# Optimization experiments

Measured on AMD Instinct MI355X. Metric: run time of the kernel, lower is better.

The kernel has to match this reference:

```python
import jax, jax.numpy as jnp
import numpy as np
import itertools

B, K, H, W = 64, 5, 320, 320
EPS = 1e-6
# All K! permutations (exact equivalent of scipy.linear_sum_assignment for KxK cost)
PERMS = np.array(list(itertools.permutations(range(K))), dtype=np.int32)  # [P, K]


def setup_inputs() -> dict:
    key = jax.random.key(0)
    k1, k2, k3 = jax.random.split(key, 3)
    return {
        "fg_logits": jax.random.normal(k1, (B, 1, H, W), dtype=jnp.float32),
        "slot_logits": jax.random.normal(k2, (B, K, H, W), dtype=jnp.float32),
        "target": jax.random.uniform(k3, (B, 1, H, W), dtype=jnp.float32),
    }


def reference(fg_logits, slot_logits, target):
    fg = target[:, 0]            # [B,H,W]
    bg = 1.0 - fg                # [B,H,W]
    # targets_b: index 0 = FG mask, 1..K-1 = BG mask (duplicated)  -> [B,K,H,W]
    targets = jnp.concatenate([fg[:, None], jnp.broadcast_to(bg[:, None], (B, K - 1, H, W))], axis=1)

    # IoU cost matrix on detached sigmoid probs (matches .detach())
    probs = jax.lax.stop_gradient(jax.nn.sigmoid(slot_logits))
    s = probs.reshape(B, K, -1)        # [B,K,N]
    t = targets.reshape(B, K, -1)      # [B,K,N]
    inter = jnp.einsum('bkn,bjn->bkj', s, t)           # [B,K,K]
    union = s.sum(-1)[:, :, None] + t.sum(-1)[:, None, :] - inter + EPS
    cost = 1.0 - inter / union                          # [B,K,K]

    # Exact Hungarian via brute force over K! permutations (K small)
    perms = jnp.asarray(PERMS)                          # [P,K]
    rows = jnp.arange(K)[None, :]                       # [1,K]
    perm_cost = cost[:, rows, perms].sum(-1)            # [B,P]
    best_perm = perms[jnp.argmin(perm_cost, axis=1)]    # [B,K] col_ind per sample

    # aligned[i] = targets[col_ind[i]]; targets[j] is fg iff j == 0
    is_fg = (best_perm == 0)[:, :, None, None]          # [B,K,1,1]
    aligned = jnp.where(is_fg, fg[:, None], bg[:, None])  # [B,K,H,W]

    # Stable sigmoid-BCE with logits, mean-reduced per sample then averaged over B
    x = slot_logits
    bce = jnp.maximum(x, 0.0) - x * aligned + jnp.log1p(jnp.exp(-jnp.abs(x)))
    return bce.mean()
```

## Files before the change

kernel.cpp:

```cpp
#include <hip/hip_runtime.h>


#define BB 64
#define KK 5
#define NPIX 102400
#define QUARTERS 4
#define SEG 25600
#define ITERS 25
#define THREADS 256
#define REC 8
#define NBLK (BB * KK * QUARTERS)

__global__ void hung_pass1(const float* __restrict__ slot,
                           const float* __restrict__ tgt,
                           float* __restrict__ ws)
{
    const int bid = blockIdx.x;
    const int q   = bid & (QUARTERS - 1);
    const int bk  = bid >> 2;
    const int b   = bk / KK;

    const float* xk = slot + (size_t)bk * NPIX + q * SEG;
    const float* t  = tgt  + (size_t)b  * NPIX + q * SEG;

    float X = 0.f, XF = 0.f, S = 0.f, SF = 0.f, PX = 0.f, Tf = 0.f;

    const int base = threadIdx.x * 4;
    #pragma unroll 5
    for (int i = 0; i < ITERS; ++i) {
        const int off = base + i * (THREADS * 4);
        const float4 fg4 = *reinterpret_cast<const float4*>(t  + off);
        const float4 x4  = *reinterpret_cast<const float4*>(xk + off);
        const float fgv[4] = {fg4.x, fg4.y, fg4.z, fg4.w};
        const float xv[4]  = {x4.x, x4.y, x4.z, x4.w};
        #pragma unroll
        for (int j = 0; j < 4; ++j) {
            const float x  = xv[j];
            const float fg = fgv[j];
            const float e  = __expf(-fabsf(x));
            const float L  = __logf(1.0f + e);
            const float d  = L + fmaxf(-x, 0.0f);
            const float s  = __expf(-d);
            PX += d;
            X  += x;
            XF  = fmaf(x, fg, XF);
            S  += s;
            SF  = fmaf(s, fg, SF);
            Tf += fg;
        }
    }

    float v[6] = {X, XF, S, SF, PX, Tf};
    #pragma unroll
    for (int j = 0; j < 6; ++j) {
        float x = v[j];
        #pragma unroll
        for (int off = 32; off > 0; off >>= 1) x += __shfl_down(x, off, 64);
        v[j] = x;
    }
    __shared__ float red[THREADS / 64][6];
    const int lane = threadIdx.x & 63;
    const int w    = threadIdx.x >> 6;
    if (lane == 0) {
        #pragma unroll
        for (int j = 0; j < 6; ++j) red[w][j] = v[j];
    }
    __syncthreads();
    if (threadIdx.x < 6) {
        const int j = threadIdx.x;
        ws[(size_t)bid * REC + j] =
            red[0][j] + red[1][j] + red[2][j] + red[3][j];
    }
}

__global__ __launch_bounds__(320) void hung_pass2(const float* __restrict__ ws,
                                                  float* __restrict__ out)
{
    __shared__ float red[BB][KK][6];
    const int t = threadIdx.x;
    if (t < BB * KK) {
        float v[6] = {0, 0, 0, 0, 0, 0};
        #pragma unroll
        for (int q = 0; q < QUARTERS; ++q) {
            const float* p = ws + (size_t)(t * QUARTERS + q) * REC;
            #pragma unroll
            for (int j = 0; j < 6; ++j) v[j] += p[j];
        }
        const int b = t / KK, k = t - b * KK;
        #pragma unroll
        for (int j = 0; j < 6; ++j) red[b][k][j] = v[j];
    }
    __syncthreads();
    if (t < BB) {
        const int b = t;
        const float Tf = red[b][0][5];
        const float Tb = (float)NPIX - Tf;
        float best = 3.402823466e+38f; int kb = 0;
        float xfsum = 0.f, px = 0.f;
        #pragma unroll
        for (int k = 0; k < KK; ++k) {
            const float Sv = red[b][k][2], Iv = red[b][k][3];
            const float cf = 1.f - Iv / (Sv + Tf - Iv + 1e-6f);
            const float Ib = Sv - Iv;
            const float cb = 1.f - Ib / (Sv + Tb - Ib + 1e-6f);
            const float dd = cf - cb;
            if (dd < best) { best = dd; kb = k; }
            xfsum += red[b][k][1];
            px    += red[b][k][4];
        }
        float res = px + xfsum - (2.f * red[b][kb][1] - red[b][kb][0]);
        #pragma unroll
        for (int off = 32; off > 0; off >>= 1) res += __shfl_down(res, off, 64);
        if (b == 0) out[0] = res * (1.0f / 32768000.0f);
    }
}

extern "C" void kernel_launch(void* const* d_in, const int* in_sizes, int n_in,
                              void* d_out, int out_size, void* d_ws, size_t ws_size,
                              hipStream_t stream) {
    const float* slot = (const float*)d_in[1];
    const float* tgt  = (const float*)d_in[2];
    float* out = (float*)d_out;
    float* ws  = (float*)d_ws;

    hung_pass1<<<NBLK, THREADS, 0, stream>>>(slot, tgt, ws);
    hung_pass2<<<1, 320, 0, stream>>>(ws, out);
}
```

Measured before the change: 222.7 us.

## Software-pipeline loads with register double buffering, nontemporal loads, cheaper sigmoid

Splits each (b,k) row into five segments instead of four. Inside each block, the next tile of slot and target vectors is prefetched into registers while the current one is computed, and slot logits are read with nontemporal loads. The sigmoid is now built from the existing exp plus a hardware reciprocal instead of a second exp. The intent is to hide memory latency and shorten the transcendental chain, at the cost of more registers. The last iteration issues redundant wrap-around loads.

```diff
diff --git a/kernel.cpp b/kernel.cpp
--- a/kernel.cpp
+++ b/kernel.cpp
@@ -4,49 +4,65 @@
 #define BB 64
 #define KK 5
 #define NPIX 102400
-#define QUARTERS 4
-#define SEG 25600
-#define ITERS 25
+#define NSEG 5
+#define SEG 20480
 #define THREADS 256
+#define INNER 4
+#define OUTER 5
 #define REC 8
-#define NBLK (BB * KK * QUARTERS)
+#define NBLK (BB * KK * NSEG)
+
+typedef float v4f __attribute__((ext_vector_type(4)));
 
 __global__ void hung_pass1(const float* __restrict__ slot,
                            const float* __restrict__ tgt,
                            float* __restrict__ ws)
 {
     const int bid = blockIdx.x;
-    const int q   = bid & (QUARTERS - 1);
-    const int bk  = bid >> 2;
+    const int q   = bid % NSEG;
+    const int bk  = bid / NSEG;
     const int b   = bk / KK;
 
     const float* xk = slot + (size_t)bk * NPIX + q * SEG;
     const float* t  = tgt  + (size_t)b  * NPIX + q * SEG;
+    const int tid4  = threadIdx.x * 4;
 
     float X = 0.f, XF = 0.f, S = 0.f, SF = 0.f, PX = 0.f, Tf = 0.f;
 
-    const int base = threadIdx.x * 4;
-    #pragma unroll 5
-    for (int i = 0; i < ITERS; ++i) {
-        const int off = base + i * (THREADS * 4);
-        const float4 fg4 = *reinterpret_cast<const float4*>(t  + off);
-        const float4 x4  = *reinterpret_cast<const float4*>(xk + off);
-        const float fgv[4] = {fg4.x, fg4.y, fg4.z, fg4.w};
-        const float xv[4]  = {x4.x, x4.y, x4.z, x4.w};
+    v4f fgB[INNER], xB[INNER];
+    #pragma unroll
+    for (int j = 0; j < INNER; ++j) {
+        const int off = (j * THREADS) * 4 + tid4;
+        fgB[j] = *reinterpret_cast<const v4f*>(t + off);
+        xB[j]  = __builtin_nontemporal_load(reinterpret_cast<const v4f*>(xk + off));
+    }
+
+    for (int o = 0; o < OUTER; ++o) {
+        const int onext = (o + 1 < OUTER) ? o + 1 : 0;
+        const int nbase = onext * (INNER * THREADS * 4) + tid4;
         #pragma unroll
-        for (int j = 0; j < 4; ++j) {
-            const float x  = xv[j];
-            const float fg = fgv[j];
-            const float e  = __expf(-fabsf(x));
-            const float L  = __logf(1.0f + e);
-            const float d  = L + fmaxf(-x, 0.0f);
-            const float s  = __expf(-d);
-            PX += d;
-            X  += x;
-            XF  = fmaf(x, fg, XF);
-            S  += s;
-            SF  = fmaf(s, fg, SF);
-            Tf += fg;
+        for (int j = 0; j < INNER; ++j) {
+            const v4f fg4 = fgB[j];
+            const v4f x4  = xB[j];
+            const int noff = nbase + j * (THREADS * 4);
+            fgB[j] = *reinterpret_cast<const v4f*>(t + noff);
+            xB[j]  = __builtin_nontemporal_load(reinterpret_cast<const v4f*>(xk + noff));
+            #pragma unroll
+            for (int u = 0; u < 4; ++u) {
+                const float x  = x4[u];
+                const float fg = fg4[u];
+                const float e  = __expf(-fabsf(x));
+                const float qq = 1.0f + e;
+                const float r  = __builtin_amdgcn_rcpf(qq);
+                const float d  = __logf(qq) + fmaxf(-x, 0.0f);
+                const float s  = (x >= 0.0f) ? r : e * r;
+                PX += d;
+                X  += x;
+                XF  = fmaf(x, fg, XF);
+                S  += s;
+                SF  = fmaf(s, fg, SF);
+                Tf += fg;
+            }
         }
     }
 
@@ -81,8 +97,8 @@
     if (t < BB * KK) {
         float v[6] = {0, 0, 0, 0, 0, 0};
         #pragma unroll
-        for (int q = 0; q < QUARTERS; ++q) {
-            const float* p = ws + (size_t)(t * QUARTERS + q) * REC;
+        for (int q = 0; q < NSEG; ++q) {
+            const float* p = ws + (size_t)(t * NSEG + q) * REC;
             #pragma unroll
             for (int j = 0; j < 6; ++j) v[j] += p[j];
         }
```

Result: no change. 223.2 us (+0.2%).
